# Kernel optimization log

Measured on AMD Instinct MI355X. Metric: run time of the kernel, lower is better.

Reference implementation:

```python
import jax, jax.numpy as jnp
import numpy as np

N = 32768      # nodes
DIN = 256      # in_channels (space dim; hyperbolic input has DIN+1 dims)
DOUT = 256     # out_channels
H = 8          # num_heads
K = 1.0        # Lorentz curvature manifold.k
P = 2          # power_k
EPS = 1e-6


def _lorentz(key, n, d):
    # random point on Lorentz manifold: time = sqrt(||space||^2 + k)
    s = jax.random.normal(key, (n, d), jnp.float32)
    t = jnp.sqrt(jnp.sum(s * s, -1, keepdims=True) + K)
    return jnp.concatenate([t, s], -1)


def setup_inputs() -> dict:
    key = jax.random.key(0)
    ks = jax.random.split(key, 8)
    sc = 0.02
    return {
        "query_input": _lorentz(ks[0], N, DIN),
        "source_input": _lorentz(ks[1], N, DIN),
        "Wq_w": jax.random.normal(ks[2], (H, DOUT, DIN + 1), jnp.float32) * sc,
        "Wq_b": jnp.zeros((H, DOUT), jnp.float32),
        "Wk_w": jax.random.normal(ks[3], (H, DOUT, DIN + 1), jnp.float32) * sc,
        "Wk_b": jnp.zeros((H, DOUT), jnp.float32),
        "Wv_w": jax.random.normal(ks[4], (H, DOUT, DIN + 1), jnp.float32) * sc,
        "Wv_b": jnp.zeros((H, DOUT), jnp.float32),
        "norm_scale": jnp.ones((), jnp.float32),
        "v_map_w": jax.random.normal(ks[5], (DOUT, DIN), jnp.float32) * sc,
        "v_map_b": jnp.zeros((DOUT,), jnp.float32),
        "final_w": jax.random.normal(ks[6], (DOUT, H * DOUT), jnp.float32) * sc,
        "final_b": jnp.zeros((DOUT,), jnp.float32),
    }


def _hyp_linear(x, W, b):
    # HypLinear for all heads at once. x: [N, Din+1], W: [H, Dout, Din+1], b: [H, Dout]
    xs = jnp.einsum('ni,hoi->nho', x, W) + b              # space part [N,H,Dout]
    xt = jnp.sqrt(jnp.sum(xs * xs, -1, keepdims=True) + K)  # Lorentz time
    return jnp.concatenate([xt, xs], -1)                  # [N,H,Dout+1]


def _fp(x, p=P):
    # fp(x) = ||x|| / ||x^p|| * x^p  (per-vector rescaled power map)
    norm_x = jnp.linalg.norm(x, axis=-1, keepdims=True)
    xp = x ** p
    norm_xp = jnp.linalg.norm(xp, axis=-1, keepdims=True)
    return norm_x / norm_xp * xp


def reference(query_input, source_input, Wq_w, Wq_b, Wk_w, Wk_b, Wv_w, Wv_b,
              norm_scale, v_map_w, v_map_b, final_w, final_b):
    q = _hyp_linear(query_input, Wq_w, Wq_b)    # [N,H,D+1]
    k = _hyp_linear(source_input, Wk_w, Wk_b)   # [N,H,D+1]
    v = _hyp_linear(source_input, Wv_w, Wv_b)   # [N,H,D+1]

    # linear_focus_attention: drop time dim
    qs, ks_, vs = q[..., 1:], k[..., 1:], v[..., 1:]     # [N,H,D]
    dscale = jnp.abs(norm_scale) + EPS
    phi_q = _fp((jax.nn.relu(qs) + EPS) / dscale)
    phi_k = _fp((jax.nn.relu(ks_) + EPS) / dscale)

    ktv = jnp.einsum('nhm,nhd->hmd', phi_k, vs)          # [H,D,D]
    numerator = jnp.einsum('nhm,hmd->nhd', phi_q, ktv)   # [N,H,D]
    denominator = jnp.einsum('nhd,hd->nh', phi_q, jnp.sum(phi_k, 0))[..., None]
    attn = numerator / (denominator + EPS)

    vss = vs @ v_map_w.T + v_map_b                       # v_map_mlp(v)
    attn = attn + vss

    # trans_heads_concat -> final_linear
    out = attn.reshape(N, H * DOUT) @ final_w.T + final_b  # [N,Dout]

    # lift back to Lorentz manifold
    t = jnp.sqrt(jnp.sum(out * out, -1, keepdims=True) + K)
    return jnp.concatenate([t, out], -1)                 # [N,Dout+1]
```

## Files before the change

kernel.cpp:

```cpp
#include <hip/hip_runtime.h>
#include <hip/hip_bf16.h>


#define EPSF 1e-6f

typedef __attribute__((ext_vector_type(8))) short bf16x8;
typedef __attribute__((ext_vector_type(8))) unsigned short u16x8;
typedef __attribute__((ext_vector_type(4))) float f32x4;
typedef float f32x4a __attribute__((ext_vector_type(4), aligned(4)));

#define STRIPE 131072

__device__ __forceinline__ float b2f(unsigned short u) {
    union { unsigned int i; float f; } c;
    c.i = ((unsigned int)u) << 16;
    return c.f;
}
__device__ __forceinline__ unsigned short f2b(float f) {
    __hip_bfloat16 h = __float2bfloat16(f);
    union { __hip_bfloat16 h; unsigned short u; } c;
    c.h = h;
    return c.u;
}

__global__ void zero_kernel(float* __restrict__ p, int n) {
    int i = blockIdx.x * 256 + threadIdx.x;
    if (i < n) p[i] = 0.f;
}

__global__ __launch_bounds__(256) void wconv_kernel(
    const float* __restrict__ Wq, const float* __restrict__ Wk, const float* __restrict__ Wv,
    const float* __restrict__ Bq, const float* __restrict__ Bk, const float* __restrict__ Bv,
    unsigned short* __restrict__ Wbf, float* __restrict__ biasAll)
{
    const int t = threadIdx.x;
    const int b = blockIdx.x;
    if (b < 6144) {
        const int mat = b >> 11, lr = b & 2047;
        const float* Ws = (mat == 0 ? Wq : mat == 1 ? Wk : Wv) + (size_t)lr * 257;
        Wbf[(size_t)b * 288 + t] = f2b(Ws[t]);
        if (t < 32) {
            float v = (t == 0) ? Ws[256] : 0.f;
            Wbf[(size_t)b * 288 + 256 + t] = f2b(v);
        }
    } else {
        const int e = (b - 6144) * 256 + t;
        const int mat = e >> 11, r = e & 2047;
        biasAll[e] = (mat == 0 ? Bq : mat == 1 ? Bk : Bv)[r];
    }
}

__global__ __launch_bounds__(256) void w2g_kernel(
    const float* __restrict__ vmw,
    const float* __restrict__ fw,
    float* __restrict__ G32)
{
    const int t = threadIdx.x;
    const int h = blockIdx.x >> 3;
    const int i0 = (blockIdx.x & 7) * 32;

    __shared__ __align__(16) float xlds[16][40];
    __shared__ float wlds[256][17];

    float acc[32];
#pragma unroll
    for (int r = 0; r < 32; ++r) acc[r] = 0.f;

    const int ar = t >> 3;
    const int ak = (t & 7) * 2;
    const int wk = t & 15;
    const int wo = (t >> 4) * 16;

    for (int d0 = 0; d0 < 256; d0 += 16) {
        xlds[ak][ar]     = vmw[(size_t)(d0 + ak) * 256 + i0 + ar];
        xlds[ak + 1][ar] = vmw[(size_t)(d0 + ak + 1) * 256 + i0 + ar];
#pragma unroll
        for (int j = 0; j < 16; ++j)
            wlds[wo + j][wk] = fw[(size_t)(wo + j) * 2048 + h * 256 + d0 + wk];
        __syncthreads();
#pragma unroll
        for (int kk = 0; kk < 16; ++kk) {
            float bv = wlds[t][kk];
            const float4* xr = (const float4*)(&xlds[kk][0]);
#pragma unroll
            for (int g = 0; g < 8; ++g) {
                float4 xv = xr[g];
                acc[g * 4 + 0] = fmaf(xv.x, bv, acc[g * 4 + 0]);
                acc[g * 4 + 1] = fmaf(xv.y, bv, acc[g * 4 + 1]);
                acc[g * 4 + 2] = fmaf(xv.z, bv, acc[g * 4 + 2]);
                acc[g * 4 + 3] = fmaf(xv.w, bv, acc[g * 4 + 3]);
            }
        }
        __syncthreads();
    }
#pragma unroll
    for (int r = 0; r < 32; ++r)
        G32[(size_t)t * 2048 + h * 256 + i0 + r] = acc[r];
}

__global__ __launch_bounds__(256) void bias2_kernel(
    const float* __restrict__ vmb, const float* __restrict__ fw,
    const float* __restrict__ fb, const float* __restrict__ Bv,
    const float* __restrict__ G32, float* __restrict__ bias2)
{
    const int o = blockIdx.x;
    const int t = threadIdx.x;
    float s = 0.f, sb = 0.f;
#pragma unroll
    for (int i = 0; i < 8; ++i) {
        const int j = t + i * 256;
        s += fw[(size_t)o * 2048 + j];
        sb += Bv[j] * G32[(size_t)o * 2048 + j];
    }
    s = s * vmb[t] + sb;
#pragma unroll
    for (int off = 32; off > 0; off >>= 1) s += __shfl_down(s, off, 64);
    __shared__ float r4[4];
    if ((t & 63) == 0) r4[t >> 6] = s;
    __syncthreads();
    if (t == 0) bias2[o] = fb[o] + r4[0] + r4[1] + r4[2] + r4[3];
}

__global__ __launch_bounds__(256) void gm_kernel(
    const float* __restrict__ Wv, const float* __restrict__ G32,
    float* __restrict__ Mf32)
{
    __shared__ float Gt[64][33];
    __shared__ float Wt[32][33];
    const int t = threadIdx.x;
    const int o0 = blockIdx.x * 64, i0 = blockIdx.y * 32, k0 = blockIdx.z * 256;
    const int ii = t & 31, og = t >> 5;
    float acc[8] = {};
    for (int kk0 = k0; kk0 < k0 + 256; kk0 += 32) {
#pragma unroll
        for (int r = 0; r < 8; ++r) {
            const int e = t + r * 256;
            Gt[e >> 5][e & 31] = G32[(size_t)(o0 + (e >> 5)) * 2048 + kk0 + (e & 31)];
        }
#pragma unroll
        for (int r = 0; r < 4; ++r) {
            const int e = t + r * 256;
            const int kk = e >> 5, i = i0 + (e & 31);
            Wt[kk][e & 31] = (i < 257) ? Wv[(size_t)(kk0 + kk) * 257 + i] : 0.f;
        }
        __syncthreads();
#pragma unroll
        for (int kk = 0; kk < 32; ++kk) {
            float wv_ = Wt[kk][ii];
#pragma unroll
            for (int r = 0; r < 8; ++r)
                acc[r] = fmaf(Gt[og * 8 + r][kk], wv_, acc[r]);
        }
        __syncthreads();
    }
#pragma unroll
    for (int r = 0; r < 8; ++r)
        atomicAdd(&Mf32[(size_t)(o0 + og * 8 + r) * 288 + i0 + ii], acc[r]);
}

__global__ void gmcvt_kernel(const float* __restrict__ Mf32, unsigned short* __restrict__ Mbf) {
    const int i = blockIdx.x * 256 + threadIdx.x;
    Mbf[i] = f2b(Mf32[i]);
}

__global__ __launch_bounds__(256) void proj_all(
    int pass,
    const float* __restrict__ X,
    const unsigned short* __restrict__ Wbf,
    const unsigned short* __restrict__ Mbf,
    const float* __restrict__ biasAll,
    unsigned short* __restrict__ phiOut,
    unsigned short* __restrict__ vsOut,
    float* __restrict__ xOut,
    const float* __restrict__ nsc,
    const float* __restrict__ colsum_in,
    float* __restrict__ colrep,
    int CH)
{
    __shared__ __align__(16) unsigned short smem[16896];
    __shared__ float reds2[4][64];
    __shared__ float reds4[4][64];
    __shared__ float rowv[64];
    __shared__ float rowx[64];
    unsigned short* lA = smem;
    unsigned short* lB = smem + 64 * 40;

    const int t = threadIdx.x;
    const int m0 = blockIdx.x * 64;
    const int y  = blockIdx.y;
    const int lane = t & 63, w = t >> 6;
    const int wn = w * 64;
    const int l15 = lane & 15, q = lane >> 4;
    const int ar = t >> 2, akg = (t & 3) * 8;

    int mode, hcol;
    const unsigned short* Wb;
    const float* bb;
    if (pass == 1)   { mode = 3; hcol = y * 256; Wb = Wbf + (size_t)hcol * 288;                bb = biasAll + hcol; }
    else if (y < 8)  { mode = 0; hcol = y * 256; Wb = Wbf + (size_t)(2048 + hcol) * 288;       bb = biasAll + 2048 + hcol; }
    else if (y < 16) { mode = 1; hcol = (y - 8) * 256; Wb = Wbf + (size_t)(4096 + hcol) * 288; bb = biasAll + 4096 + hcol; }
    else             { mode = 2; hcol = 0; Wb = Mbf; bb = nullptr; }

    f32x4 acc[4][4] = {};
    const float* XA = X + (size_t)(m0 + ar) * 257 + akg;
    const unsigned short* WB = Wb + (size_t)ar * 288 + akg;

    f32x4a cx0, cx1;
    u16x8 cw[4];
    cx0 = *(const f32x4a*)(XA);
    cx1 = *(const f32x4a*)(XA + 4);
#pragma unroll
    for (int qq = 0; qq < 4; ++qq)
        cw[qq] = *(const u16x8*)(WB + (size_t)qq * 64 * 288);

    for (int ks = 0; ks < 8; ++ks) {
        {
            u16x8 pk;
            pk[0] = f2b(cx0[0]); pk[1] = f2b(cx0[1]);
            pk[2] = f2b(cx0[2]); pk[3] = f2b(cx0[3]);
            pk[4] = f2b(cx1[0]); pk[5] = f2b(cx1[1]);
            pk[6] = f2b(cx1[2]); pk[7] = f2b(cx1[3]);
            *(u16x8*)(&lA[ar * 40 + akg]) = pk;
        }
#pragma unroll
        for (int qq = 0; qq < 4; ++qq)
            *(u16x8*)(&lB[(ar + qq * 64) * 40 + akg]) = cw[qq];
        if (ks < 7) {
            const int k1 = (ks + 1) * 32;
            cx0 = *(const f32x4a*)(XA + k1);
            cx1 = *(const f32x4a*)(XA + k1 + 4);
#pragma unroll
            for (int qq = 0; qq < 4; ++qq)
                cw[qq] = *(const u16x8*)(WB + (size_t)qq * 64 * 288 + k1);
        }
        __syncthreads();
        bf16x8 af[4], bfr[4];
#pragma unroll
        for (int i = 0; i < 4; ++i)
            af[i] = *(const bf16x8*)(&lA[(i * 16 + l15) * 40 + q * 8]);
#pragma unroll
        for (int j = 0; j < 4; ++j)
            bfr[j] = *(const bf16x8*)(&lB[(wn + j * 16 + l15) * 40 + q * 8]);
#pragma unroll
        for (int i = 0; i < 4; ++i)
#pragma unroll
            for (int j = 0; j < 4; ++j)
                acc[i][j] = __builtin_amdgcn_mfma_f32_16x16x32_bf16(af[i], bfr[j], acc[i][j], 0, 0, 0);
        __syncthreads();
    }

    if (t < 64) rowx[t] = b2f(f2b(X[(size_t)(m0 + t) * 257 + 256]));
    __syncthreads();

    {
        float w256[4];
#pragma unroll
        for (int j = 0; j < 4; ++j)
            w256[j] = b2f(Wb[(size_t)(wn + j * 16 + l15) * 288 + 256]);
#pragma unroll
        for (int i = 0; i < 4; ++i)
#pragma unroll
            for (int r = 0; r < 4; ++r) {
                const float xv = rowx[i * 16 + q * 4 + r];
#pragma unroll
                for (int j = 0; j < 4; ++j)
                    acc[i][j][r] += xv * w256[j];
            }
    }

    if (mode == 2) {
#pragma unroll
        for (int j = 0; j < 4; ++j) {
            const int cg = wn + j * 16 + l15;
#pragma unroll
            for (int i = 0; i < 4; ++i)
#pragma unroll
                for (int r = 0; r < 4; ++r) {
                    const int n = m0 + i * 16 + q * 4 + r;
                    xOut[(size_t)n * 257 + 1 + cg] = acc[i][j][r];
                }
        }
        return;
    }

    if (mode == 1) {
#pragma unroll
        for (int j = 0; j < 4; ++j) {
            const float bias = bb[wn + j * 16 + l15];
#pragma unroll
            for (int i = 0; i < 4; ++i)
#pragma unroll
                for (int r = 0; r < 4; ++r)
                    acc[i][j][r] += bias;
        }
#pragma unroll
        for (int i = 0; i < 4; ++i)
#pragma unroll
            for (int j = 0; j < 4; ++j) {
                const int cl = wn + j * 16 + l15;
#pragma unroll
                for (int r2 = 0; r2 < 4; r2 += 2) {
                    const int nl = i * 16 + q * 4 + r2;
                    const unsigned int pk =
                        (unsigned int)f2b(acc[i][j][r2]) |
                        ((unsigned int)f2b(acc[i][j][r2 + 1]) << 16);
                    *(unsigned int*)(&smem[cl * 64 + (((nl >> 3) ^ (cl & 7)) << 3) + (nl & 7)]) = pk;
                }
            }
        __syncthreads();
#pragma unroll
        for (int k = 0; k < 8; ++k) {
            const int task = k * 256 + t;
            const int cl = task >> 3, nq = task & 7;
            *(u16x8*)(vsOut + (size_t)blockIdx.x * STRIPE +
                      (size_t)(hcol + cl) * 64 + nq * 8) =
                *(const u16x8*)(&smem[cl * 64 + ((nq ^ (cl & 7)) << 3)]);
        }
        return;
    }

    const float c = fabsf(nsc[0]) + EPSF;
    float bias[4];
#pragma unroll
    for (int j = 0; j < 4; ++j) bias[j] = bb[wn + j * 16 + l15];

    float a2[4][4], a4[4][4];
#pragma unroll
    for (int i = 0; i < 4; ++i)
#pragma unroll
        for (int r = 0; r < 4; ++r) { a2[i][r] = 0.f; a4[i][r] = 0.f; }
#pragma unroll
    for (int i = 0; i < 4; ++i)
#pragma unroll
        for (int j = 0; j < 4; ++j)
#pragma unroll
            for (int r = 0; r < 4; ++r) {
                float uu = fmaxf(acc[i][j][r] + bias[j], 0.f) + EPSF;
                float q2 = uu * uu;
                acc[i][j][r] = q2;
                a2[i][r] += q2;
                a4[i][r] += q2 * q2;
            }
#pragma unroll
    for (int m = 1; m <= 8; m <<= 1) {
#pragma unroll
        for (int i = 0; i < 4; ++i)
#pragma unroll
            for (int r = 0; r < 4; ++r) {
                a2[i][r] += __shfl_xor(a2[i][r], m, 64);
                a4[i][r] += __shfl_xor(a4[i][r], m, 64);
            }
    }
    if (l15 == 0) {
#pragma unroll
        for (int i = 0; i < 4; ++i)
#pragma unroll
            for (int r = 0; r < 4; ++r) {
                reds2[w][i * 16 + q * 4 + r] = a2[i][r];
                reds4[w][i * 16 + q * 4 + r] = a4[i][r];
            }
    }
    __syncthreads();
    if (t < 64) {
        float s2t = reds2[0][t] + reds2[1][t] + reds2[2][t] + reds2[3][t];
        float s4t = reds4[0][t] + reds4[1][t] + reds4[2][t] + reds4[3][t];
        rowv[t] = sqrtf(s2t) / (c * sqrtf(s4t));
    }
    __syncthreads();
    float sc_[4][4];
#pragma unroll
    for (int i = 0; i < 4; ++i)
#pragma unroll
        for (int r = 0; r < 4; ++r) sc_[i][r] = rowv[i * 16 + q * 4 + r];

    if (mode == 0) {
        float colp[4];
#pragma unroll
        for (int j = 0; j < 4; ++j) colp[j] = 0.f;
#pragma unroll
        for (int i = 0; i < 4; ++i)
#pragma unroll
            for (int j = 0; j < 4; ++j)
#pragma unroll
                for (int r = 0; r < 4; ++r) {
                    float ph = acc[i][j][r] * sc_[i][r];
                    acc[i][j][r] = ph;
                    colp[j] += ph;
                }
#pragma unroll
        for (int i = 0; i < 4; ++i)
#pragma unroll
            for (int j = 0; j < 4; ++j) {
                const int cl = wn + j * 16 + l15;
#pragma unroll
                for (int r2 = 0; r2 < 4; r2 += 2) {
                    const int nl = i * 16 + q * 4 + r2;
                    const unsigned int pk =
                        (unsigned int)f2b(acc[i][j][r2]) |
                        ((unsigned int)f2b(acc[i][j][r2 + 1]) << 16);
                    *(unsigned int*)(&smem[cl * 64 + (((nl >> 3) ^ (cl & 7)) << 3) + (nl & 7)]) = pk;
                }
            }
        __syncthreads();
#pragma unroll
        for (int k = 0; k < 8; ++k) {
            const int task = k * 256 + t;
            const int cl = task >> 3, nq = task & 7;
            *(u16x8*)(phiOut + (size_t)blockIdx.x * STRIPE +
                      (size_t)(hcol + cl) * 64 + nq * 8) =
                *(const u16x8*)(&smem[cl * 64 + ((nq ^ (cl & 7)) << 3)]);
        }
#pragma unroll
        for (int j = 0; j < 4; ++j) {
            colp[j] += __shfl_xor(colp[j], 16, 64);
            colp[j] += __shfl_xor(colp[j], 32, 64);
        }
        if (q == 0) {
            float* dst = colrep + (size_t)(blockIdx.x & 7) * 2048;
#pragma unroll
            for (int j = 0; j < 4; ++j)
                atomicAdd(&dst[hcol + wn + j * 16 + l15], colp[j]);
        }
    } else {
        float cs[4];
#pragma unroll
        for (int j = 0; j < 4; ++j) cs[j] = colsum_in[hcol + wn + j * 16 + l15];
        float dp[4][4];
#pragma unroll
        for (int i = 0; i < 4; ++i)
#pragma unroll
            for (int r = 0; r < 4; ++r) dp[i][r] = 0.f;
#pragma unroll
        for (int i = 0; i < 4; ++i)
#pragma unroll
            for (int j = 0; j < 4; ++j)
#pragma unroll
                for (int r = 0; r < 4; ++r) {
                    float ph = acc[i][j][r] * sc_[i][r];
                    acc[i][j][r] = ph;
                    dp[i][r] += ph * cs[j];
                }
#pragma unroll
        for (int m = 1; m <= 8; m <<= 1) {
#pragma unroll
            for (int i = 0; i < 4; ++i)
#pragma unroll
                for (int r = 0; r < 4; ++r)
                    dp[i][r] += __shfl_xor(dp[i][r], m, 64);
        }
        if (l15 == 0) {
#pragma unroll
            for (int i = 0; i < 4; ++i)
#pragma unroll
                for (int r = 0; r < 4; ++r)
                    reds2[w][i * 16 + q * 4 + r] = dp[i][r];
        }
        __syncthreads();
        if (t < 64) {
            float dt = reds2[0][t] + reds2[1][t] + reds2[2][t] + reds2[3][t];
            rowv[t] = 1.f / (dt + EPSF);
        }
        __syncthreads();
#pragma unroll
        for (int i = 0; i < 4; ++i)
#pragma unroll
            for (int r = 0; r < 4; ++r) sc_[i][r] = rowv[i * 16 + q * 4 + r];
#pragma unroll
        for (int i = 0; i < 4; ++i)
#pragma unroll
            for (int j = 0; j < 4; ++j) {
                const int cl = wn + j * 16 + l15;
#pragma unroll
                for (int r = 0; r < 4; ++r) {
                    const int nl = i * 16 + q * 4 + r;
                    smem[nl * 264 + cl] = f2b(acc[i][j][r] * sc_[i][r]);
                }
            }
        __syncthreads();
#pragma unroll
        for (int k = 0; k < 8; ++k) {
            const int task = k * 256 + t;
            const int rowl = task >> 5, ck = (task & 31) * 8;
            *(u16x8*)(phiOut + (size_t)(m0 + rowl) * 2048 + hcol + ck) =
                *(const u16x8*)(&smem[rowl * 264 + ck]);
        }
    }
}

__global__ __launch_bounds__(256) void merge_colsum(
    const float* __restrict__ rep, float* __restrict__ out)
{
    const int cidx = blockIdx.x * 256 + threadIdx.x;
    float s = 0.f;
#pragma unroll
    for (int r = 0; r < 8; ++r) s += rep[(size_t)r * 2048 + cidx];
    out[cidx] = s;
}

__global__ __launch_bounds__(256) void ktv_mfma(
    const unsigned short* __restrict__ phiT,
    const unsigned short* __restrict__ vsT,
    float* __restrict__ ktv, int CH)
{
    __shared__ __align__(16) unsigned short lAT[128 * 64];
    __shared__ __align__(16) unsigned short lBT[128 * 64];
    const int t = threadIdx.x;
    const int h = blockIdx.y;
    const int split = blockIdx.x >> 2;
    const int tile = blockIdx.x & 3;
    const int m0 = (tile >> 1) * 128, d0 = (tile & 1) * 128;
    const int chh = h * 256;
    const int lane = t & 63, w = t >> 6;
    const int wm = (w >> 1) * 64, wn = (w & 1) * 64;
    const int l15 = lane & 15, q = lane >> 4;
    const int sl7 = l15 & 7;

    const int scg  = t >> 3;
    const int snq  = t & 7;
    const int sbase = scg * 64 + ((snq ^ (scg & 7)) << 3);

    f32x4 acc[4][4] = {};
    const int st0 = split * 8;

    const unsigned short* pA = phiT + (size_t)(chh + m0 + scg) * 64 + snq * 8;
    const unsigned short* pB = vsT  + (size_t)(chh + d0 + scg) * 64 + snq * 8;

    u16x8 cA[4], cB[4], nA[4], nB[4];
#pragma unroll
    for (int k = 0; k < 4; ++k) {
        cA[k] = *(const u16x8*)(pA + (size_t)st0 * STRIPE + k * 2048);
        cB[k] = *(const u16x8*)(pB + (size_t)st0 * STRIPE + k * 2048);
    }

    for (int it = 0; it < 8; ++it) {
#pragma unroll
        for (int k = 0; k < 4; ++k) {
            *(u16x8*)(&lAT[k * 2048 + sbase]) = cA[k];
            *(u16x8*)(&lBT[k * 2048 + sbase]) = cB[k];
        }
        if (it < 7) {
            const size_t so = (size_t)(st0 + it + 1) * STRIPE;
#pragma unroll
            for (int k = 0; k < 4; ++k) {
                nA[k] = *(const u16x8*)(pA + so + k * 2048);
                nB[k] = *(const u16x8*)(pB + so + k * 2048);
            }
        }
        __syncthreads();
#pragma unroll
        for (int sub = 0; sub < 2; ++sub) {
            const int slot = ((sub * 4 + q) ^ sl7) << 3;
            bf16x8 af[4], bfr[4];
#pragma unroll
            for (int i = 0; i < 4; ++i)
                af[i] = *(const bf16x8*)(&lAT[(wm + i * 16 + l15) * 64 + slot]);
#pragma unroll
            for (int j = 0; j < 4; ++j)
                bfr[j] = *(const bf16x8*)(&lBT[(wn + j * 16 + l15) * 64 + slot]);
#pragma unroll
            for (int i = 0; i < 4; ++i)
#pragma unroll
                for (int j = 0; j < 4; ++j)
                    acc[i][j] = __builtin_amdgcn_mfma_f32_16x16x32_bf16(af[i], bfr[j], acc[i][j], 0, 0, 0);
        }
        __syncthreads();
        if (it < 7) {
#pragma unroll
            for (int k = 0; k < 4; ++k) { cA[k] = nA[k]; cB[k] = nB[k]; }
        }
    }
#pragma unroll
    for (int i = 0; i < 4; ++i)
#pragma unroll
        for (int j = 0; j < 4; ++j)
#pragma unroll
            for (int r = 0; r < 4; ++r) {
                const int m = m0 + wm + i * 16 + q * 4 + r;
                const int d = d0 + wn + j * 16 + l15;
                atomicAdd(&ktv[((size_t)chh + m) * 256 + d], acc[i][j][r]);
            }
}

__device__ __forceinline__ void fin_load(
    const unsigned short* __restrict__ Abuf, const unsigned short* __restrict__ W2T,
    int n0, int d0, int t, int k0,
    u16x8& A0, u16x8& A1, u16x8& B)
{
    {
        const int row = t >> 2, kg = (t & 3) * 8;
        A0 = *(const u16x8*)(Abuf + (size_t)(n0 + row) * 2048 + ((k0 + kg) & 2047));
    }
    {
        const int e = t + 256;
        const int row = e >> 2, kg = (e & 3) * 8;
        A1 = *(const u16x8*)(Abuf + (size_t)(n0 + row) * 2048 + ((k0 + kg) & 2047));
    }
    {
        const int row = t >> 2, kg = (t & 3) * 8;
        B = *(const u16x8*)(W2T + (size_t)(d0 + row) * 4096 + k0 + kg);
    }
}

__global__ __launch_bounds__(256) void final_mfma(
    const unsigned short* __restrict__ Abuf,
    const unsigned short* __restrict__ W2T,
    int kbeg, int kend,
    float* __restrict__ outp)
{
    __shared__ __align__(16) unsigned short lA[128 * 40];
    __shared__ __align__(16) unsigned short lB[64 * 40];
    const int t = threadIdx.x;
    const int n0 = blockIdx.x * 128;
    const int d0 = blockIdx.y * 64;
    const int khalf = (kend - kbeg) >> 1;
    const int kb = kbeg + blockIdx.z * khalf;
    const int ke = kb + khalf;
    const int lane = t & 63, w = t >> 6;
    const int wm = w * 32;
    const int l15 = lane & 15, q = lane >> 4;

    f32x4 acc[2][4] = {};
    u16x8 cA0, cA1, cB, nA0, nA1, nB;
    fin_load(Abuf, W2T, n0, d0, t, kb, cA0, cA1, cB);

    for (int k0 = kb; k0 < ke; k0 += 32) {
        {
            const int row = t >> 2, kg = (t & 3) * 8;
            *(u16x8*)(&lA[row * 40 + kg]) = cA0;
            *(u16x8*)(&lB[row * 40 + kg]) = cB;
        }
        {
            const int e = t + 256;
            const int row = e >> 2, kg = (e & 3) * 8;
            *(u16x8*)(&lA[row * 40 + kg]) = cA1;
        }
        if (k0 + 32 < ke)
            fin_load(Abuf, W2T, n0, d0, t, k0 + 32, nA0, nA1, nB);
        __syncthreads();
        bf16x8 af[2], bfr[4];
#pragma unroll
        for (int i = 0; i < 2; ++i)
            af[i] = *(const bf16x8*)(&lA[(wm + i * 16 + l15) * 40 + q * 8]);
#pragma unroll
        for (int j = 0; j < 4; ++j)
            bfr[j] = *(const bf16x8*)(&lB[(j * 16 + l15) * 40 + q * 8]);
#pragma unroll
        for (int i = 0; i < 2; ++i)
#pragma unroll
            for (int j = 0; j < 4; ++j)
                acc[i][j] = __builtin_amdgcn_mfma_f32_16x16x32_bf16(af[i], bfr[j], acc[i][j], 0, 0, 0);
        __syncthreads();
        if (k0 + 32 < ke) { cA0 = nA0; cA1 = nA1; cB = nB; }
    }
#pragma unroll
    for (int i = 0; i < 2; ++i)
#pragma unroll
        for (int j = 0; j < 4; ++j)
#pragma unroll
            for (int r = 0; r < 4; ++r) {
                const int n = n0 + wm + i * 16 + q * 4 + r;
                const int d = d0 + j * 16 + l15;
                atomicAdd(&outp[(size_t)n * 257 + 1 + d], acc[i][j][r]);
            }
}

__global__ __launch_bounds__(256) void w2u_kernel(
    const float* __restrict__ ktv,
    const float* __restrict__ fw,
    unsigned short* __restrict__ W2T)
{
    const int t = threadIdx.x;
    const int h = blockIdx.x >> 3;
    const int m0 = (blockIdx.x & 7) * 32;

    __shared__ __align__(16) float xlds[16][40];
    __shared__ float wlds[256][17];

    float acc[32];
#pragma unroll
    for (int r = 0; r < 32; ++r) acc[r] = 0.f;

    const int ar = t >> 3;
    const int ak = (t & 7) * 2;
    const int wk = t & 15;
    const int wo = (t >> 4) * 16;

    for (int d0 = 0; d0 < 256; d0 += 16) {
        {
            const float* src = ktv + (size_t)(h * 256 + m0 + ar) * 256 + d0 + ak;
            xlds[ak][ar]     = src[0];
            xlds[ak + 1][ar] = src[1];
        }
#pragma unroll
        for (int j = 0; j < 16; ++j)
            wlds[wo + j][wk] = fw[(size_t)(wo + j) * 2048 + h * 256 + d0 + wk];
        __syncthreads();
#pragma unroll
        for (int kk = 0; kk < 16; ++kk) {
            float bv = wlds[t][kk];
            const float4* xr = (const float4*)(&xlds[kk][0]);
#pragma unroll
            for (int g = 0; g < 8; ++g) {
                float4 xv = xr[g];
                acc[g * 4 + 0] = fmaf(xv.x, bv, acc[g * 4 + 0]);
                acc[g * 4 + 1] = fmaf(xv.y, bv, acc[g * 4 + 1]);
                acc[g * 4 + 2] = fmaf(xv.z, bv, acc[g * 4 + 2]);
                acc[g * 4 + 3] = fmaf(xv.w, bv, acc[g * 4 + 3]);
            }
        }
        __syncthreads();
    }
#pragma unroll
    for (int r = 0; r < 32; ++r)
        W2T[(size_t)t * 4096 + h * 256 + m0 + r] = f2b(acc[r]);
}

__global__ __launch_bounds__(256) void lift_kernel(
    const float* __restrict__ bias2, float* __restrict__ outp)
{
    const int t = threadIdx.x;
    const int lane = t & 63;
    const int w = t >> 6;
    const int n0 = blockIdx.x * 64 + w * 16;
    float b[4];
#pragma unroll
    for (int j = 0; j < 4; ++j) b[j] = bias2[lane + j * 64];
    for (int r = 0; r < 16; ++r) {
        float* row = outp + (size_t)(n0 + r) * 257;
        float v[4];
        float s = 0.f;
#pragma unroll
        for (int j = 0; j < 4; ++j) {
            v[j] = row[1 + lane + j * 64] + b[j];
            s = fmaf(v[j], v[j], s);
        }
#pragma unroll
        for (int off = 32; off > 0; off >>= 1) s += __shfl_down(s, off, 64);
#pragma unroll
        for (int j = 0; j < 4; ++j) row[1 + lane + j * 64] = v[j];
        if (lane == 0) row[0] = sqrtf(s + 1.0f);
    }
}

extern "C" void kernel_launch(void* const* d_in, const int* in_sizes, int n_in,
                              void* d_out, int out_size, void* d_ws, size_t ws_size,
                              hipStream_t stream)
{
    const float* xq  = (const float*)d_in[0];
    const float* xs  = (const float*)d_in[1];
    const float* Wq  = (const float*)d_in[2];
    const float* Bq  = (const float*)d_in[3];
    const float* Wk  = (const float*)d_in[4];
    const float* Bk  = (const float*)d_in[5];
    const float* Wv  = (const float*)d_in[6];
    const float* Bv  = (const float*)d_in[7];
    const float* nsc = (const float*)d_in[8];
    const float* vmw = (const float*)d_in[9];
    const float* vmb = (const float*)d_in[10];
    const float* fw  = (const float*)d_in[11];
    const float* fb  = (const float*)d_in[12];
    float* outp = (float*)d_out;

    char* ws = (char*)d_ws;
    float* ktv          = (float*)(ws + 0);
    float* colrep       = (float*)(ws + 2097152);
    float* Mf32         = (float*)(ws + 2162688);
    float* colsum       = (float*)(ws + 2457600);
    float* bias2        = (float*)(ws + 2465792);
    float* biasAll      = (float*)(ws + 2466816);
    unsigned short* W2T = (unsigned short*)(ws + 2491392);
    unsigned short* Wbf = (unsigned short*)(ws + 4588544);
    float* G32          = (float*)(ws + 8127488);
    unsigned short* Mbf = (unsigned short*)(ws + 10224640);
    const size_t fixedBytes = 10372096;

    int CH = 2048;
    if      (ws_size >= fixedBytes + (size_t)32768 * 8192) CH = 32768;
    else if (ws_size >= fixedBytes + (size_t)16384 * 8192) CH = 16384;
    else if (ws_size >= fixedBytes + (size_t)8192 * 8192)  CH = 8192;
    else if (ws_size >= fixedBytes + (size_t)4096 * 8192)  CH = 4096;
    const int NCHK = 32768 / CH;
    unsigned short* phibuf = (unsigned short*)(ws + fixedBytes);
    unsigned short* vsT    = (unsigned short*)(ws + fixedBytes + (size_t)CH * 4096);

    zero_kernel<<<dim3(2400), 256, 0, stream>>>(ktv, 614400);
    wconv_kernel<<<dim3(6168), 256, 0, stream>>>(Wq, Wk, Wv, Bq, Bk, Bv, Wbf, biasAll);
    w2g_kernel<<<dim3(64), 256, 0, stream>>>(vmw, fw, G32);
    bias2_kernel<<<dim3(256), 256, 0, stream>>>(vmb, fw, fb, Bv, G32, bias2);
    gm_kernel<<<dim3(4, 9, 8), 256, 0, stream>>>(Wv, G32, Mf32);
    gmcvt_kernel<<<dim3(288), 256, 0, stream>>>(Mf32, Mbf);

    for (int c = 0; c < NCHK; ++c) {
        const float* xs_c = xs + (size_t)c * CH * 257;
        float* out_c = outp + (size_t)c * CH * 257;
        proj_all<<<dim3(CH / 64, 17), 256, 0, stream>>>(
            0, xs_c, Wbf, Mbf, biasAll, phibuf, vsT, out_c,
            nsc, nullptr, colrep, CH);
        ktv_mfma<<<dim3((CH / 512) * 4, 8), 256, 0, stream>>>(phibuf, vsT, ktv, CH);
    }

    merge_colsum<<<dim3(8), 256, 0, stream>>>(colrep, colsum);
    w2u_kernel<<<dim3(64), 256, 0, stream>>>(ktv, fw, W2T);

    for (int c = 0; c < NCHK; ++c) {
        const float* xq_c = xq + (size_t)c * CH * 257;
        float* out_c = outp + (size_t)c * CH * 257;
        proj_all<<<dim3(CH / 64, 8), 256, 0, stream>>>(
            1, xq_c, Wbf, Mbf, biasAll, phibuf, vsT, out_c,
            nsc, colsum, nullptr, CH);
        final_mfma<<<dim3(CH / 128, 4, 2), 256, 0, stream>>>(phibuf, W2T, 0, 2048, out_c);
    }

    lift_kernel<<<dim3(512), 256, 0, stream>>>(bias2, outp);
}
```

Baseline: 1.049 ms.

## Split projection kernel per pass, double-buffer LDS staging, cap chunk size

```diff
diff --git a/kernel.cpp b/kernel.cpp
--- a/kernel.cpp
+++ b/kernel.cpp
@@ -163,8 +163,31 @@
     Mbf[i] = f2b(Mf32[i]);
 }
 
-__global__ __launch_bounds__(256) void proj_all(
-    int pass,
+__device__ __forceinline__ void stage_load(
+    const float* __restrict__ XA, const unsigned short* __restrict__ WB, int k,
+    f32x4a& cx0, f32x4a& cx1, u16x8 cw[4])
+{
+    cx0 = *(const f32x4a*)(XA + k);
+    cx1 = *(const f32x4a*)(XA + k + 4);
+#pragma unroll
+    for (int qq = 0; qq < 4; ++qq)
+        cw[qq] = *(const u16x8*)(WB + (size_t)qq * 64 * 288 + k);
+}
+
+__device__ __forceinline__ void stage_write(
+    unsigned short* __restrict__ la, unsigned short* __restrict__ lb,
+    int ar, int akg, f32x4a cx0, f32x4a cx1, const u16x8 cw[4])
+{
+    u16x8 pk;
+    pk[0] = f2b(cx0[0]); pk[1] = f2b(cx0[1]); pk[2] = f2b(cx0[2]); pk[3] = f2b(cx0[3]);
+    pk[4] = f2b(cx1[0]); pk[5] = f2b(cx1[1]); pk[6] = f2b(cx1[2]); pk[7] = f2b(cx1[3]);
+    *(u16x8*)(&la[ar * 40 + akg]) = pk;
+#pragma unroll
+    for (int qq = 0; qq < 4; ++qq)
+        *(u16x8*)(&lb[(ar + qq * 64) * 40 + akg]) = cw[qq];
+}
+
+__global__ __launch_bounds__(256, 3) void proj_all(
     const float* __restrict__ X,
     const unsigned short* __restrict__ Wbf,
     const unsigned short* __restrict__ Mbf,
@@ -173,8 +196,250 @@
     unsigned short* __restrict__ vsOut,
     float* __restrict__ xOut,
     const float* __restrict__ nsc,
+    float* __restrict__ colrep,
+    int CH)
+{
+    __shared__ __align__(16) unsigned short smem[25600];
+    float* reds2 = (float*)(smem + 16896);
+    float* reds4 = reds2 + 256;
+    float* rowv  = reds4 + 256;
+    float* rowx  = rowv + 64;
+
+    const int t = threadIdx.x;
+    const int m0 = blockIdx.x * 64;
+    const int y  = blockIdx.y;
+    const int lane = t & 63, w = t >> 6;
+    const int wn = w * 64;
+    const int l15 = lane & 15, q = lane >> 4;
+    const int ar = t >> 2, akg = (t & 3) * 8;
+
+    int mode, hcol;
+    const unsigned short* Wb;
+    const float* bb;
+    if (y < 8)       { mode = 0; hcol = y * 256; Wb = Wbf + (size_t)(2048 + hcol) * 288;       bb = biasAll + 2048 + hcol; }
+    else if (y < 16) { mode = 1; hcol = (y - 8) * 256; Wb = Wbf + (size_t)(4096 + hcol) * 288; bb = biasAll + 4096 + hcol; }
+    else             { mode = 2; hcol = 0; Wb = Mbf; bb = nullptr; }
+
+    f32x4 acc[4][4] = {};
+    const float* XA = X + (size_t)(m0 + ar) * 257 + akg;
+    const unsigned short* WB = Wb + (size_t)ar * 288 + akg;
+
+    f32x4a cx0, cx1;
+    u16x8 cw[4];
+
+    stage_load(XA, WB, 0, cx0, cx1, cw);
+    stage_write(smem, smem + 5120, ar, akg, cx0, cx1, cw);
+    stage_load(XA, WB, 32, cx0, cx1, cw);
+    __syncthreads();
+
+#pragma unroll
+    for (int ks = 0; ks < 8; ++ks) {
+        const int b = ks & 1;
+        unsigned short* la = smem + (b ? 2560 : 0);
+        unsigned short* lb = smem + (b ? 15360 : 5120);
+        bf16x8 af[4], bfr[4];
+#pragma unroll
+        for (int i = 0; i < 4; ++i)
+            af[i] = *(const bf16x8*)(&la[(i * 16 + l15) * 40 + q * 8]);
+#pragma unroll
+        for (int j = 0; j < 4; ++j)
+            bfr[j] = *(const bf16x8*)(&lb[(wn + j * 16 + l15) * 40 + q * 8]);
+#pragma unroll
+        for (int i = 0; i < 4; ++i)
+#pragma unroll
+            for (int j = 0; j < 4; ++j)
+                acc[i][j] = __builtin_amdgcn_mfma_f32_16x16x32_bf16(af[i], bfr[j], acc[i][j], 0, 0, 0);
+        if (ks < 7) {
+            unsigned short* la2 = smem + (b ? 0 : 2560);
+            unsigned short* lb2 = smem + (b ? 5120 : 15360);
+            stage_write(la2, lb2, ar, akg, cx0, cx1, cw);
+            if (ks < 6) stage_load(XA, WB, (ks + 2) * 32, cx0, cx1, cw);
+        }
+        __syncthreads();
+    }
+
+    if (t < 64) rowx[t] = b2f(f2b(X[(size_t)(m0 + t) * 257 + 256]));
+    __syncthreads();
+
+    {
+        float w256[4];
+#pragma unroll
+        for (int j = 0; j < 4; ++j)
+            w256[j] = b2f(Wb[(size_t)(wn + j * 16 + l15) * 288 + 256]);
+#pragma unroll
+        for (int i = 0; i < 4; ++i)
+#pragma unroll
+            for (int r = 0; r < 4; ++r) {
+                const float xv = rowx[i * 16 + q * 4 + r];
+#pragma unroll
+                for (int j = 0; j < 4; ++j)
+                    acc[i][j][r] += xv * w256[j];
+            }
+    }
+
+    if (mode == 2) {
+#pragma unroll
+        for (int j = 0; j < 4; ++j) {
+            const int cg = wn + j * 16 + l15;
+#pragma unroll
+            for (int i = 0; i < 4; ++i)
+#pragma unroll
+                for (int r = 0; r < 4; ++r) {
+                    const int n = m0 + i * 16 + q * 4 + r;
+                    xOut[(size_t)n * 257 + 1 + cg] = acc[i][j][r];
+                }
+        }
+        return;
+    }
+
+    if (mode == 1) {
+#pragma unroll
+        for (int j = 0; j < 4; ++j) {
+            const float bias = bb[wn + j * 16 + l15];
+#pragma unroll
+            for (int i = 0; i < 4; ++i)
+#pragma unroll
+                for (int r = 0; r < 4; ++r)
+                    acc[i][j][r] += bias;
+        }
+        __syncthreads();
+#pragma unroll
+        for (int i = 0; i < 4; ++i)
+#pragma unroll
+            for (int j = 0; j < 4; ++j) {
+                const int cl = wn + j * 16 + l15;
+#pragma unroll
+                for (int r2 = 0; r2 < 4; r2 += 2) {
+                    const int nl = i * 16 + q * 4 + r2;
+                    const unsigned int pk =
+                        (unsigned int)f2b(acc[i][j][r2]) |
+                        ((unsigned int)f2b(acc[i][j][r2 + 1]) << 16);
+                    *(unsigned int*)(&smem[cl * 64 + (((nl >> 3) ^ (cl & 7)) << 3) + (nl & 7)]) = pk;
+                }
+            }
+        __syncthreads();
+#pragma unroll
+        for (int k = 0; k < 8; ++k) {
+            const int task = k * 256 + t;
+            const int cl = task >> 3, nq = task & 7;
+            *(u16x8*)(vsOut + (size_t)blockIdx.x * STRIPE +
+                      (size_t)(hcol + cl) * 64 + nq * 8) =
+                *(const u16x8*)(&smem[cl * 64 + ((nq ^ (cl & 7)) << 3)]);
+        }
+        return;
+    }
+
+    const float c = fabsf(nsc[0]) + EPSF;
+    float bias[4];
+#pragma unroll
+    for (int j = 0; j < 4; ++j) bias[j] = bb[wn + j * 16 + l15];
+
+    float a2[4][4], a4[4][4];
+#pragma unroll
+    for (int i = 0; i < 4; ++i)
+#pragma unroll
+        for (int r = 0; r < 4; ++r) { a2[i][r] = 0.f; a4[i][r] = 0.f; }
+#pragma unroll
+    for (int i = 0; i < 4; ++i)
+#pragma unroll
+        for (int j = 0; j < 4; ++j)
+#pragma unroll
+            for (int r = 0; r < 4; ++r) {
+                float uu = fmaxf(acc[i][j][r] + bias[j], 0.f) + EPSF;
+                float q2 = uu * uu;
+                acc[i][j][r] = q2;
+                a2[i][r] += q2;
+                a4[i][r] += q2 * q2;
+            }
+#pragma unroll
+    for (int m = 1; m <= 8; m <<= 1) {
+#pragma unroll
+        for (int i = 0; i < 4; ++i)
+#pragma unroll
+            for (int r = 0; r < 4; ++r) {
+                a2[i][r] += __shfl_xor(a2[i][r], m, 64);
+                a4[i][r] += __shfl_xor(a4[i][r], m, 64);
+            }
+    }
+    __syncthreads();
+    if (l15 == 0) {
+#pragma unroll
+        for (int i = 0; i < 4; ++i)
+#pragma unroll
+            for (int r = 0; r < 4; ++r) {
+                reds2[w * 64 + i * 16 + q * 4 + r] = a2[i][r];
+                reds4[w * 64 + i * 16 + q * 4 + r] = a4[i][r];
+            }
+    }
+    __syncthreads();
+    if (t < 64) {
+        float s2t = reds2[t] + reds2[64 + t] + reds2[128 + t] + reds2[192 + t];
+        float s4t = reds4[t] + reds4[64 + t] + reds4[128 + t] + reds4[192 + t];
+        rowv[t] = sqrtf(s2t) / (c * sqrtf(s4t));
+    }
+    __syncthreads();
+    float sc_[4][4];
+#pragma unroll
+    for (int i = 0; i < 4; ++i)
+#pragma unroll
+        for (int r = 0; r < 4; ++r) sc_[i][r] = rowv[i * 16 + q * 4 + r];
+
+    float colp[4];
+#pragma unroll
+    for (int j = 0; j < 4; ++j) colp[j] = 0.f;
+#pragma unroll
+    for (int i = 0; i < 4; ++i)
+#pragma unroll
+        for (int j = 0; j < 4; ++j)
+#pragma unroll
+            for (int r = 0; r < 4; ++r) {
+                float ph = acc[i][j][r] * sc_[i][r];
+                acc[i][j][r] = ph;
+                colp[j] += ph;
+            }
+#pragma unroll
+    for (int i = 0; i < 4; ++i)
+#pragma unroll
+        for (int j = 0; j < 4; ++j) {
+            const int cl = wn + j * 16 + l15;
+#pragma unroll
+            for (int r2 = 0; r2 < 4; r2 += 2) {
+                const int nl = i * 16 + q * 4 + r2;
+                const unsigned int pk =
+                    (unsigned int)f2b(acc[i][j][r2]) |
+                    ((unsigned int)f2b(acc[i][j][r2 + 1]) << 16);
+                *(unsigned int*)(&smem[cl * 64 + (((nl >> 3) ^ (cl & 7)) << 3) + (nl & 7)]) = pk;
+            }
+        }
+    __syncthreads();
+#pragma unroll
+    for (int k = 0; k < 8; ++k) {
+        const int task = k * 256 + t;
+        const int cl = task >> 3, nq = task & 7;
+        *(u16x8*)(phiOut + (size_t)blockIdx.x * STRIPE +
+                  (size_t)(hcol + cl) * 64 + nq * 8) =
+            *(const u16x8*)(&smem[cl * 64 + ((nq ^ (cl & 7)) << 3)]);
+    }
+#pragma unroll
+    for (int j = 0; j < 4; ++j) {
+        colp[j] += __shfl_xor(colp[j], 16, 64);
+        colp[j] += __shfl_xor(colp[j], 32, 64);
+    }
+    if (q == 0) {
+        float* dst = colrep + (size_t)(blockIdx.x & 7) * 2048;
+#pragma unroll
+        for (int j = 0; j < 4; ++j)
+            atomicAdd(&dst[hcol + wn + j * 16 + l15], colp[j]);
+    }
+}
+
+__global__ __launch_bounds__(256) void proj_phi(
+    const float* __restrict__ X,
+    const unsigned short* __restrict__ Wbase,
+    const float* __restrict__ biasBase,
+    unsigned short* __restrict__ outbuf,
+    const float* __restrict__ nsc,
     const float* __restrict__ colsum_in,
-    float* __restrict__ colrep,
     int CH)
 {
     __shared__ __align__(16) unsigned short smem[16896];
@@ -187,23 +452,15 @@
 
     const int t = threadIdx.x;
     const int m0 = blockIdx.x * 64;
-    const int y  = blockIdx.y;
+    const int h  = blockIdx.y;
     const int lane = t & 63, w = t >> 6;
     const int wn = w * 64;
     const int l15 = lane & 15, q = lane >> 4;
     const int ar = t >> 2, akg = (t & 3) * 8;
 
-    int mode, hcol;
-    const unsigned short* Wb;
-    const float* bb;
-    if (pass == 1)   { mode = 3; hcol = y * 256; Wb = Wbf + (size_t)hcol * 288;                bb = biasAll + hcol; }
-    else if (y < 8)  { mode = 0; hcol = y * 256; Wb = Wbf + (size_t)(2048 + hcol) * 288;       bb = biasAll + 2048 + hcol; }
-    else if (y < 16) { mode = 1; hcol = (y - 8) * 256; Wb = Wbf + (size_t)(4096 + hcol) * 288; bb = biasAll + 4096 + hcol; }
-    else             { mode = 2; hcol = 0; Wb = Mbf; bb = nullptr; }
-
     f32x4 acc[4][4] = {};
     const float* XA = X + (size_t)(m0 + ar) * 257 + akg;
-    const unsigned short* WB = Wb + (size_t)ar * 288 + akg;
+    const unsigned short* WB = Wbase + (size_t)(h * 256 + ar) * 288 + akg;
 
     f32x4a cx0, cx1;
     u16x8 cw[4];
@@ -256,7 +513,7 @@
         float w256[4];
 #pragma unroll
         for (int j = 0; j < 4; ++j)
-            w256[j] = b2f(Wb[(size_t)(wn + j * 16 + l15) * 288 + 256]);
+            w256[j] = b2f(Wbase[(size_t)(h * 256 + wn + j * 16 + l15) * 288 + 256]);
 #pragma unroll
         for (int i = 0; i < 4; ++i)
 #pragma unroll
@@ -268,61 +525,10 @@
             }
     }
 
-    if (mode == 2) {
-#pragma unroll
-        for (int j = 0; j < 4; ++j) {
-            const int cg = wn + j * 16 + l15;
-#pragma unroll
-            for (int i = 0; i < 4; ++i)
-#pragma unroll
-                for (int r = 0; r < 4; ++r) {
-                    const int n = m0 + i * 16 + q * 4 + r;
-                    xOut[(size_t)n * 257 + 1 + cg] = acc[i][j][r];
-                }
-        }
-        return;
-    }
-
-    if (mode == 1) {
-#pragma unroll
-        for (int j = 0; j < 4; ++j) {
-            const float bias = bb[wn + j * 16 + l15];
-#pragma unroll
-            for (int i = 0; i < 4; ++i)
-#pragma unroll
-                for (int r = 0; r < 4; ++r)
-                    acc[i][j][r] += bias;
-        }
-#pragma unroll
-        for (int i = 0; i < 4; ++i)
-#pragma unroll
-            for (int j = 0; j < 4; ++j) {
-                const int cl = wn + j * 16 + l15;
-#pragma unroll
-                for (int r2 = 0; r2 < 4; r2 += 2) {
-                    const int nl = i * 16 + q * 4 + r2;
-                    const unsigned int pk =
-                        (unsigned int)f2b(acc[i][j][r2]) |
-                        ((unsigned int)f2b(acc[i][j][r2 + 1]) << 16);
-                    *(unsigned int*)(&smem[cl * 64 + (((nl >> 3) ^ (cl & 7)) << 3) + (nl & 7)]) = pk;
-                }
-            }
-        __syncthreads();
-#pragma unroll
-        for (int k = 0; k < 8; ++k) {
-            const int task = k * 256 + t;
-            const int cl = task >> 3, nq = task & 7;
-            *(u16x8*)(vsOut + (size_t)blockIdx.x * STRIPE +
-                      (size_t)(hcol + cl) * 64 + nq * 8) =
-                *(const u16x8*)(&smem[cl * 64 + ((nq ^ (cl & 7)) << 3)]);
-        }
-        return;
-    }
-
     const float c = fabsf(nsc[0]) + EPSF;
     float bias[4];
 #pragma unroll
-    for (int j = 0; j < 4; ++j) bias[j] = bb[wn + j * 16 + l15];
+    for (int j = 0; j < 4; ++j) bias[j] = biasBase[h * 256 + wn + j * 16 + l15];
 
     float a2[4][4], a4[4][4];
 #pragma unroll
@@ -373,117 +579,67 @@
 #pragma unroll
         for (int r = 0; r < 4; ++r) sc_[i][r] = rowv[i * 16 + q * 4 + r];
 
-    if (mode == 0) {
-        float colp[4];
-#pragma unroll
-        for (int j = 0; j < 4; ++j) colp[j] = 0.f;
-#pragma unroll
-        for (int i = 0; i < 4; ++i)
-#pragma unroll
-            for (int j = 0; j < 4; ++j)
-#pragma unroll
-                for (int r = 0; r < 4; ++r) {
-                    float ph = acc[i][j][r] * sc_[i][r];
-                    acc[i][j][r] = ph;
-                    colp[j] += ph;
-                }
-#pragma unroll
-        for (int i = 0; i < 4; ++i)
-#pragma unroll
-            for (int j = 0; j < 4; ++j) {
-                const int cl = wn + j * 16 + l15;
-#pragma unroll
-                for (int r2 = 0; r2 < 4; r2 += 2) {
-                    const int nl = i * 16 + q * 4 + r2;
-                    const unsigned int pk =
-                        (unsigned int)f2b(acc[i][j][r2]) |
-                        ((unsigned int)f2b(acc[i][j][r2 + 1]) << 16);
-                    *(unsigned int*)(&smem[cl * 64 + (((nl >> 3) ^ (cl & 7)) << 3) + (nl & 7)]) = pk;
-                }
-            }
-        __syncthreads();
-#pragma unroll
-        for (int k = 0; k < 8; ++k) {
-            const int task = k * 256 + t;
-            const int cl = task >> 3, nq = task & 7;
-            *(u16x8*)(phiOut + (size_t)blockIdx.x * STRIPE +
-                      (size_t)(hcol + cl) * 64 + nq * 8) =
-                *(const u16x8*)(&smem[cl * 64 + ((nq ^ (cl & 7)) << 3)]);
-        }
+    float cs[4];
+#pragma unroll
+    for (int j = 0; j < 4; ++j) cs[j] = colsum_in[h * 256 + wn + j * 16 + l15];
+    float dp[4][4];
+#pragma unroll
+    for (int i = 0; i < 4; ++i)
+#pragma unroll
+        for (int r = 0; r < 4; ++r) dp[i][r] = 0.f;
+#pragma unroll
+    for (int i = 0; i < 4; ++i)
+#pragma unroll
+        for (int j = 0; j < 4; ++j)
+#pragma unroll
+            for (int r = 0; r < 4; ++r) {
+                float ph = acc[i][j][r] * sc_[i][r];
+                acc[i][j][r] = ph;
+                dp[i][r] += ph * cs[j];
+            }
+#pragma unroll
+    for (int m = 1; m <= 8; m <<= 1) {
+#pragma unroll
+        for (int i = 0; i < 4; ++i)
+#pragma unroll
+            for (int r = 0; r < 4; ++r)
+                dp[i][r] += __shfl_xor(dp[i][r], m, 64);
+    }
+    if (l15 == 0) {
+#pragma unroll
+        for (int i = 0; i < 4; ++i)
+#pragma unroll
+            for (int r = 0; r < 4; ++r)
+                reds2[w][i * 16 + q * 4 + r] = dp[i][r];
+    }
+    __syncthreads();
+    if (t < 64) {
+        float dt = reds2[0][t] + reds2[1][t] + reds2[2][t] + reds2[3][t];
+        rowv[t] = 1.f / (dt + EPSF);
+    }
+    __syncthreads();
+#pragma unroll
+    for (int i = 0; i < 4; ++i)
+#pragma unroll
+        for (int r = 0; r < 4; ++r) sc_[i][r] = rowv[i * 16 + q * 4 + r];
+#pragma unroll
+    for (int i = 0; i < 4; ++i)
 #pragma unroll
         for (int j = 0; j < 4; ++j) {
-            colp[j] += __shfl_xor(colp[j], 16, 64);
-            colp[j] += __shfl_xor(colp[j], 32, 64);
-        }
-        if (q == 0) {
-            float* dst = colrep + (size_t)(blockIdx.x & 7) * 2048;
-#pragma unroll
-            for (int j = 0; j < 4; ++j)
-                atomicAdd(&dst[hcol + wn + j * 16 + l15], colp[j]);
-        }
-    } else {
-        float cs[4];
-#pragma unroll
-        for (int j = 0; j < 4; ++j) cs[j] = colsum_in[hcol + wn + j * 16 + l15];
-        float dp[4][4];
-#pragma unroll
-        for (int i = 0; i < 4; ++i)
-#pragma unroll
-            for (int r = 0; r < 4; ++r) dp[i][r] = 0.f;
-#pragma unroll
-        for (int i = 0; i < 4; ++i)
-#pragma unroll
-            for (int j = 0; j < 4; ++j)
-#pragma unroll
-                for (int r = 0; r < 4; ++r) {
-                    float ph = acc[i][j][r] * sc_[i][r];
-                    acc[i][j][r] = ph;
-                    dp[i][r] += ph * cs[j];
-                }
-#pragma unroll
-        for (int m = 1; m <= 8; m <<= 1) {
-#pragma unroll
-            for (int i = 0; i < 4; ++i)
-#pragma unroll
-                for (int r = 0; r < 4; ++r)
-                    dp[i][r] += __shfl_xor(dp[i][r], m, 64);
-        }
-        if (l15 == 0) {
-#pragma unroll
-            for (int i = 0; i < 4; ++i)
-#pragma unroll
-                for (int r = 0; r < 4; ++r)
-                    reds2[w][i * 16 + q * 4 + r] = dp[i][r];
-        }
-        __syncthreads();
-        if (t < 64) {
-            float dt = reds2[0][t] + reds2[1][t] + reds2[2][t] + reds2[3][t];
-            rowv[t] = 1.f / (dt + EPSF);
-        }
-        __syncthreads();
-#pragma unroll
-        for (int i = 0; i < 4; ++i)
-#pragma unroll
-            for (int r = 0; r < 4; ++r) sc_[i][r] = rowv[i * 16 + q * 4 + r];
-#pragma unroll
-        for (int i = 0; i < 4; ++i)
-#pragma unroll
-            for (int j = 0; j < 4; ++j) {
-                const int cl = wn + j * 16 + l15;
-#pragma unroll
-                for (int r = 0; r < 4; ++r) {
-                    const int nl = i * 16 + q * 4 + r;
-                    smem[nl * 264 + cl] = f2b(acc[i][j][r] * sc_[i][r]);
-                }
-            }
-        __syncthreads();
-#pragma unroll
-        for (int k = 0; k < 8; ++k) {
-            const int task = k * 256 + t;
-            const int rowl = task >> 5, ck = (task & 31) * 8;
-            *(u16x8*)(phiOut + (size_t)(m0 + rowl) * 2048 + hcol + ck) =
-                *(const u16x8*)(&smem[rowl * 264 + ck]);
-        }
+            const int cl = wn + j * 16 + l15;
+#pragma unroll
+            for (int r = 0; r < 4; ++r) {
+                const int nl = i * 16 + q * 4 + r;
+                smem[nl * 264 + cl] = f2b(acc[i][j][r] * sc_[i][r]);
+            }
+        }
+    __syncthreads();
+#pragma unroll
+    for (int k = 0; k < 8; ++k) {
+        const int task = k * 256 + t;
+        const int rowl = task >> 5, ck = (task & 31) * 8;
+        *(u16x8*)(outbuf + (size_t)(m0 + rowl) * 2048 + h * 256 + ck) =
+            *(const u16x8*)(&smem[rowl * 264 + ck]);
     }
 }
 
@@ -775,9 +931,7 @@
     const size_t fixedBytes = 10372096;
 
     int CH = 2048;
-    if      (ws_size >= fixedBytes + (size_t)32768 * 8192) CH = 32768;
-    else if (ws_size >= fixedBytes + (size_t)16384 * 8192) CH = 16384;
-    else if (ws_size >= fixedBytes + (size_t)8192 * 8192)  CH = 8192;
+    if      (ws_size >= fixedBytes + (size_t)8192 * 8192)  CH = 8192;
     else if (ws_size >= fixedBytes + (size_t)4096 * 8192)  CH = 4096;
     const int NCHK = 32768 / CH;
     unsigned short* phibuf = (unsigned short*)(ws + fixedBytes);
@@ -794,8 +948,7 @@
         const float* xs_c = xs + (size_t)c * CH * 257;
         float* out_c = outp + (size_t)c * CH * 257;
         proj_all<<<dim3(CH / 64, 17), 256, 0, stream>>>(
-            0, xs_c, Wbf, Mbf, biasAll, phibuf, vsT, out_c,
-            nsc, nullptr, colrep, CH);
+            xs_c, Wbf, Mbf, biasAll, phibuf, vsT, out_c, nsc, colrep, CH);
         ktv_mfma<<<dim3((CH / 512) * 4, 8), 256, 0, stream>>>(phibuf, vsT, ktv, CH);
     }
 
@@ -805,9 +958,8 @@
     for (int c = 0; c < NCHK; ++c) {
         const float* xq_c = xq + (size_t)c * CH * 257;
         float* out_c = outp + (size_t)c * CH * 257;
-        proj_all<<<dim3(CH / 64, 8), 256, 0, stream>>>(
-            1, xq_c, Wbf, Mbf, biasAll, phibuf, vsT, out_c,
-            nsc, colsum, nullptr, CH);
+        proj_phi<<<dim3(CH / 64, 8), 256, 0, stream>>>(
+            xq_c, Wbf, biasAll, phibuf, nsc, colsum, CH);
         final_mfma<<<dim3(CH / 128, 4, 2), 256, 0, stream>>>(phibuf, W2T, 0, 2048, out_c);
     }
 
```

After: 943.4 us. 1.11x faster.
